# Optimization experiments

Measured on AMD Instinct MI355X. Metric: run time of the kernel, lower is better.

Reference implementation:

```python
import jax, jax.numpy as jnp
import numpy as np

N = 50000
E = 800000
IN_CH = 64
HID = 32
HEADS = 8
OUT_CH = 32
NEG_SLOPE = 0.2  # PyG GATConv default leaky_relu slope


def gat_conv(x, src, dst, W, a_src, a_dst, bias, heads, out_ch, concat, n_nodes):
    # x: [N, F_in]; W: [F_in, heads*out_ch]; a_*: [heads, out_ch]; bias: [heads*out_ch] or [out_ch]
    h = (x @ W).reshape(n_nodes, heads, out_ch)            # [N, H, C]
    alpha_s = jnp.sum(h * a_src, axis=-1)                  # [N, H]
    alpha_d = jnp.sum(h * a_dst, axis=-1)                  # [N, H]
    e = jax.nn.leaky_relu(alpha_s[src] + alpha_d[dst], NEG_SLOPE)  # [E, H]
    # segment softmax over destination node
    m = jax.ops.segment_max(e, dst, num_segments=n_nodes)  # [N, H]
    ex = jnp.exp(e - m[dst])                               # [E, H]
    denom = jax.ops.segment_sum(ex, dst, num_segments=n_nodes)  # [N, H]
    alpha = ex / (denom[dst] + 1e-16)                      # [E, H]
    out = jax.ops.segment_sum(alpha[:, :, None] * h[src], dst, num_segments=n_nodes)  # [N, H, C]
    out = out.reshape(n_nodes, heads * out_ch) if concat else out.mean(axis=1)
    return out + bias


def setup_inputs() -> dict:
    key = jax.random.key(0)
    ks = jax.random.split(key, 12)
    x = jax.random.normal(ks[0], (N, IN_CH), dtype=jnp.float32)
    edge_index = jax.random.randint(ks[1], (2, E), 0, N, dtype=jnp.int32)
    s1 = 1.0 / np.sqrt(IN_CH)
    s2 = 1.0 / np.sqrt(HEADS * HID)
    W1 = jax.random.uniform(ks[2], (IN_CH, HEADS * HID), jnp.float32, -s1, s1)
    a_src1 = jax.random.uniform(ks[3], (HEADS, HID), jnp.float32, -s2, s2)
    a_dst1 = jax.random.uniform(ks[4], (HEADS, HID), jnp.float32, -s2, s2)
    b1 = jnp.zeros((HEADS * HID,), jnp.float32)
    W2 = jax.random.uniform(ks[5], (HEADS * HID, OUT_CH), jnp.float32, -s2, s2)
    a_src2 = jax.random.uniform(ks[6], (1, OUT_CH), jnp.float32, -s2, s2)
    a_dst2 = jax.random.uniform(ks[7], (1, OUT_CH), jnp.float32, -s2, s2)
    b2 = jnp.zeros((OUT_CH,), jnp.float32)
    return {"x": x, "edge_index": edge_index, "W1": W1, "a_src1": a_src1,
            "a_dst1": a_dst1, "b1": b1, "W2": W2, "a_src2": a_src2,
            "a_dst2": a_dst2, "b2": b2}


def reference(x, edge_index, W1, a_src1, a_dst1, b1, W2, a_src2, a_dst2, b2):
    # add self-loops (PyG GATConv default)
    loops = jnp.arange(N, dtype=edge_index.dtype)
    src = jnp.concatenate([edge_index[0], loops])
    dst = jnp.concatenate([edge_index[1], loops])
    h = gat_conv(x, src, dst, W1, a_src1, a_dst1, b1, HEADS, HID, True, N)
    h = jax.nn.relu(h)  # dropout inactive in eval
    out = gat_conv(h, src, dst, W2, a_src2, a_dst2, b2, 1, OUT_CH, False, N)
    return jax.nn.log_softmax(out, axis=1)
```

## Files before the change

### kernel.cpp

```cpp
#include <hip/hip_runtime.h>
#include <math.h>
#include <stdint.h>

#define NN 50000
#define NE 800000
#define INC 64
#define HEADS 8
#define F1 256
#define OC 32
#define NEGS 0.2f

#define NB 391
#define BCAP 2432
#define SCB2 125
#define G1B 1564
#define CSTR 64

typedef unsigned short ushort_t;
typedef float floatx2 __attribute__((ext_vector_type(2)));

__device__ __forceinline__ ushort_t f2bf(float f) {
    uint32_t u = __builtin_bit_cast(uint32_t, f);
    uint32_t r = (u + 0x7fffu + ((u >> 16) & 1u)) >> 16;
    return (ushort_t)r;
}
__device__ __forceinline__ float bflo(uint32_t p) { return __builtin_bit_cast(float, p << 16); }
__device__ __forceinline__ float bfhi(uint32_t p) { return __builtin_bit_cast(float, p & 0xffff0000u); }
__device__ __forceinline__ float bf2f(ushort_t v) { return __builtin_bit_cast(float, (uint32_t)v << 16); }

#if __has_builtin(__builtin_amdgcn_cvt_pk_fp8_f32) && __has_builtin(__builtin_amdgcn_cvt_pk_f32_fp8)
#define HW_FP8 1
#endif

__device__ __forceinline__ uint32_t f2e4m3_sw(float x) {
    float a = fabsf(x);
    uint32_t s = (__builtin_bit_cast(uint32_t, x) >> 31) << 7;
    if (a < 0.015625f) {
        uint32_t m = (uint32_t)rintf(a * 512.0f);
        return s | m;
    }
    if (a >= 448.f) return s | 0x7e;
    uint32_t u = __builtin_bit_cast(uint32_t, a);
    int E = (int)((u >> 23) & 255) - 127;
    float scale = __builtin_bit_cast(float, (uint32_t)(3 - E + 127) << 23);
    uint32_t q = (uint32_t)rintf(a * scale);
    if (q == 16) { E += 1; q = 8; }
    return s | ((uint32_t)(E + 7) << 3) | (q - 8);
}
__device__ __forceinline__ float e4m3f_sw(uint32_t b) {
    uint32_t e = (b >> 3) & 15, m = b & 7;
    float v;
    if (e) v = __builtin_bit_cast(float, ((e + 120u) << 23) | (m << 20));
    else   v = (float)m * 0.001953125f;
    return (b & 0x80u) ? -v : v;
}

__device__ __forceinline__ uint32_t pack4_fp8(float a, float b, float c, float d) {
#ifdef HW_FP8
    int v = __builtin_amdgcn_cvt_pk_fp8_f32(a, b, 0, false);
    v = __builtin_amdgcn_cvt_pk_fp8_f32(c, d, v, true);
    return (uint32_t)v;
#else
    return f2e4m3_sw(a) | (f2e4m3_sw(b) << 8) | (f2e4m3_sw(c) << 16) | (f2e4m3_sw(d) << 24);
#endif
}
__device__ __forceinline__ void unpack4_fp8(uint32_t r, float& f0, float& f1, float& f2, float& f3) {
#ifdef HW_FP8
    floatx2 lo = __builtin_amdgcn_cvt_pk_f32_fp8((int)r, false);
    floatx2 hi = __builtin_amdgcn_cvt_pk_f32_fp8((int)r, true);
    f0 = lo[0]; f1 = lo[1]; f2 = hi[0]; f3 = hi[1];
#else
    f0 = e4m3f_sw(r & 255); f1 = e4m3f_sw((r >> 8) & 255);
    f2 = e4m3f_sw((r >> 16) & 255); f3 = e4m3f_sw(r >> 24);
#endif
}

__global__ __launch_bounds__(256) void k_zero(int* __restrict__ gcnt) {
    int i = blockIdx.x * 256 + threadIdx.x;
    if (i < NB) gcnt[i] = 0;
}

__global__ __launch_bounds__(256) void k_gemm1(
    const float* __restrict__ x, const float* __restrict__ W1,
    const float* __restrict__ a_s, const float* __restrict__ a_d,
    uint8_t* __restrict__ h1, float* __restrict__ alpha_s, float* __restrict__ alpha_d,
    const int* __restrict__ ei, int* __restrict__ gcnt, uint32_t* __restrict__ gbuf)
{
    __shared__ float xt[INC][64];
    __shared__ uint32_t scnt_[NB];
    __shared__ uint32_t soff_[NB];
    int b = blockIdx.x;
    int t = threadIdx.x;

    if (b < SCB2) {
        for (int i = t; i < NB; i += 256) scnt_[i] = 0;
        __syncthreads();
        const int* dsts = ei + NE;
        int ebase = b * 6400;
#pragma unroll
        for (int j = 0; j < 25; ++j) {
            int d = dsts[ebase + j * 256 + t];
            atomicAdd(&scnt_[d >> 7], 1u);
        }
        __syncthreads();
        for (int i = t; i < NB; i += 256) {
            uint32_t c = scnt_[i];
            uint32_t base = 0;
            if (c) base = (uint32_t)atomicAdd(&gcnt[i], (int)c);
            if (base > BCAP) base = BCAP;
            uint32_t end = base + c; if (end > BCAP) end = BCAP;
            soff_[i] = (uint32_t)i * BCAP + base;
            scnt_[i] = (uint32_t)i * BCAP + end;
        }
        __syncthreads();
#pragma unroll
        for (int j = 0; j < 25; ++j) {
            int e = ebase + j * 256 + t;
            int s = ei[e];
            int d = dsts[e];
            int bkt = d >> 7;
            uint32_t slot = atomicAdd(&soff_[bkt], 1u);
            if (slot < scnt_[bkt])
                gbuf[slot] = ((uint32_t)(d & 127) << 16) | (uint32_t)s;
        }
        return;
    }

    int gb = b - SCB2;
    int ntile = gb >> 1;
    int hc = gb & 1;
    int nb = ntile * 64;

    {
        int n = t >> 2;
        int kq = (t & 3) << 4;
        int gn = nb + n;
        if (gn < NN) {
            const float* xr = x + (size_t)gn * INC + kq;
#pragma unroll
            for (int j = 0; j < 16; j += 4) {
                float4 v = *(const float4*)(xr + j);
                xt[kq + j + 0][n] = v.x; xt[kq + j + 1][n] = v.y;
                xt[kq + j + 2][n] = v.z; xt[kq + j + 3][n] = v.w;
            }
        } else {
#pragma unroll
            for (int j = 0; j < 16; ++j) xt[kq + j][n] = 0.f;
        }
    }
    __syncthreads();

    int lane = t & 63, w = t >> 6;
    int ng = lane >> 5;
    int c0 = (lane & 31) << 2;
    int nbase = (w << 4) + (ng << 3);
    int cglob = hc * 128 + c0;
    const float* Wp = W1 + cglob;

    float acc[8][4];
#pragma unroll
    for (int i = 0; i < 8; i++) { acc[i][0] = acc[i][1] = acc[i][2] = acc[i][3] = 0.f; }

#pragma unroll 4
    for (int k = 0; k < INC; ++k) {
        float4 wv = *(const float4*)(Wp + k * F1);
        const float4* xs = (const float4*)&xt[k][nbase];
        float4 xa = xs[0], xb = xs[1];
        float xq[8];
        xq[0] = xa.x; xq[1] = xa.y; xq[2] = xa.z; xq[3] = xa.w;
        xq[4] = xb.x; xq[5] = xb.y; xq[6] = xb.z; xq[7] = xb.w;
#pragma unroll
        for (int ns = 0; ns < 8; ++ns) {
            float xvv = xq[ns];
            acc[ns][0] = fmaf(xvv, wv.x, acc[ns][0]);
            acc[ns][1] = fmaf(xvv, wv.y, acc[ns][1]);
            acc[ns][2] = fmaf(xvv, wv.z, acc[ns][2]);
            acc[ns][3] = fmaf(xvv, wv.w, acc[ns][3]);
        }
    }

    float4 av = *(const float4*)(a_s + cglob);
    float4 dv = *(const float4*)(a_d + cglob);
    int head = hc * 4 + ((lane & 31) >> 3);
#pragma unroll
    for (int ns = 0; ns < 8; ++ns) {
        int n = nb + nbase + ns;
        if (n < NN) {
            uint32_t pk = pack4_fp8(acc[ns][0], acc[ns][1], acc[ns][2], acc[ns][3]);
            *(uint32_t*)(h1 + (size_t)n * F1 + cglob) = pk;
            float ps = acc[ns][0] * av.x + acc[ns][1] * av.y + acc[ns][2] * av.z + acc[ns][3] * av.w;
            float pd = acc[ns][0] * dv.x + acc[ns][1] * dv.y + acc[ns][2] * dv.z + acc[ns][3] * dv.w;
            ps += __shfl_xor(ps, 1); ps += __shfl_xor(ps, 2); ps += __shfl_xor(ps, 4);
            pd += __shfl_xor(pd, 1); pd += __shfl_xor(pd, 2); pd += __shfl_xor(pd, 4);
            if ((lane & 7) == 0) {
                alpha_s[n * HEADS + head] = ps;
                alpha_d[n * HEADS + head] = pd;
            }
        }
    }
}

__global__ __launch_bounds__(256) void k_transpose(
    const int* __restrict__ gcnt, const uint32_t* __restrict__ gbuf,
    ushort_t* __restrict__ csr, int* __restrict__ deg)
{
    __shared__ uint32_t cnt[128], off[128], run[128], sc[128];
    __shared__ ushort_t sent[BCAP];
    int sb = blockIdx.x;
    int t = threadIdx.x;
    if (t < 128) cnt[t] = 0;
    __syncthreads();
    int total = gcnt[sb]; if (total > BCAP) total = BCAP;
    const uint32_t* gb_ = gbuf + (size_t)sb * BCAP;

    for (int i = t; i < total; i += 256) {
        uint32_t v = gb_[i];
        atomicAdd(&cnt[v >> 16], 1u);
    }
    __syncthreads();
    if (t < 128) sc[t] = cnt[t];
    __syncthreads();
    for (int ofs = 1; ofs < 128; ofs <<= 1) {
        uint32_t v = 0;
        if (t < 128 && t >= (uint32_t)ofs) v = sc[t - ofs];
        __syncthreads();
        if (t < 128) sc[t] += v;
        __syncthreads();
    }
    if (t < 128) { off[t] = sc[t] - cnt[t]; run[t] = sc[t] - cnt[t]; }
    __syncthreads();
    for (int i = t; i < total; i += 256) {
        uint32_t v = gb_[i];
        uint32_t slot = atomicAdd(&run[v >> 16], 1u);
        sent[slot] = (ushort_t)(v & 0xffffu);
    }
    __syncthreads();
    int n = t >> 1, half = t & 1;
    int dg = (int)cnt[n];
    if (dg > CSTR) dg = CSTR;
    int d = sb * 128 + n;
    if (half == 0) deg[d] = dg;
    const ushort_t* src = sent + off[n];
    ushort_t* dst = csr + (size_t)d * CSTR;
    for (int j = half; j < dg; j += 2) dst[j] = src[j];
}

__global__ __launch_bounds__(256) void k_gather1(
    const uint8_t* __restrict__ h1,
    const float* __restrict__ alpha_s, const float* __restrict__ alpha_d,
    const int* __restrict__ deg_, const ushort_t* __restrict__ csr,
    const float* __restrict__ b1, uint8_t* __restrict__ h1r8)
{
    int wid = (blockIdx.x * blockDim.x + threadIdx.x) >> 6;
    if (wid >= NN) return;
    int lane = threadIdx.x & 63;
    int d = wid;
    int deg = deg_[d];
    const ushort_t* lst = csr + (size_t)d * CSTR;
    int hh = lane >> 3;
    int he = lane & 7;
    float ad = alpha_d[d * HEADS + hh];
    float ad8 = alpha_d[d * HEADS + he];
    int cb = lane << 2;
    const uint8_t* hbase = h1 + cb;

    float4 A0 = {0.f, 0.f, 0.f, 0.f}, A1 = {0.f, 0.f, 0.f, 0.f};
    float dn0 = 0.f, dn1 = 0.f;

    {
        float e = alpha_s[d * HEADS + hh] + ad;
        uint32_t r = *(const uint32_t*)(hbase + (size_t)d * F1);
        e = (e > 0.f) ? e : NEGS * e;
        float w = __expf(e);
        float f0, f1, f2, f3;
        unpack4_fp8(r, f0, f1, f2, f3);
        dn0 += w;
        A0.x = fmaf(w, f0, A0.x); A0.y = fmaf(w, f1, A0.y);
        A0.z = fmaf(w, f2, A0.z); A0.w = fmaf(w, f3, A0.w);
    }

    int i = 0;
    int je = lane >> 3;
    for (; i + 16 <= deg; i += 16) {
        uint4 pa = *(const uint4*)(lst + i);
        uint4 pb = *(const uint4*)(lst + i + 8);
        uint32_t pwa = (je < 4) ? ((je < 2) ? pa.x : pa.y) : ((je < 6) ? pa.z : pa.w);
        int sa = (je & 1) ? (int)(pwa >> 16) : (int)(pwa & 0xffffu);
        float eoA = alpha_s[sa * HEADS + he] + ad8;
        uint32_t pwb = (je < 4) ? ((je < 2) ? pb.x : pb.y) : ((je < 6) ? pb.z : pb.w);
        int sb_ = (je & 1) ? (int)(pwb >> 16) : (int)(pwb & 0xffffu);
        float eoB = alpha_s[sb_ * HEADS + he] + ad8;
        eoA = (eoA > 0.f) ? eoA : NEGS * eoA;
        eoB = (eoB > 0.f) ? eoB : NEGS * eoB;
        float wA = __expf(eoA);
        float wB = __expf(eoB);
        uint32_t r[16];
        r[0]  = *(const uint32_t*)(hbase + (size_t)(pa.x & 0xffffu) * F1);
        r[1]  = *(const uint32_t*)(hbase + (size_t)(pa.x >> 16) * F1);
        r[2]  = *(const uint32_t*)(hbase + (size_t)(pa.y & 0xffffu) * F1);
        r[3]  = *(const uint32_t*)(hbase + (size_t)(pa.y >> 16) * F1);
        r[4]  = *(const uint32_t*)(hbase + (size_t)(pa.z & 0xffffu) * F1);
        r[5]  = *(const uint32_t*)(hbase + (size_t)(pa.z >> 16) * F1);
        r[6]  = *(const uint32_t*)(hbase + (size_t)(pa.w & 0xffffu) * F1);
        r[7]  = *(const uint32_t*)(hbase + (size_t)(pa.w >> 16) * F1);
        r[8]  = *(const uint32_t*)(hbase + (size_t)(pb.x & 0xffffu) * F1);
        r[9]  = *(const uint32_t*)(hbase + (size_t)(pb.x >> 16) * F1);
        r[10] = *(const uint32_t*)(hbase + (size_t)(pb.y & 0xffffu) * F1);
        r[11] = *(const uint32_t*)(hbase + (size_t)(pb.y >> 16) * F1);
        r[12] = *(const uint32_t*)(hbase + (size_t)(pb.z & 0xffffu) * F1);
        r[13] = *(const uint32_t*)(hbase + (size_t)(pb.z >> 16) * F1);
        r[14] = *(const uint32_t*)(hbase + (size_t)(pb.w & 0xffffu) * F1);
        r[15] = *(const uint32_t*)(hbase + (size_t)(pb.w >> 16) * F1);
#pragma unroll
        for (int j = 0; j < 16; ++j) {
            float w = (j < 8) ? __shfl(wA, (j << 3) + hh)
                              : __shfl(wB, ((j - 8) << 3) + hh);
            float f0, f1, f2, f3;
            unpack4_fp8(r[j], f0, f1, f2, f3);
            if (j & 1) {
                dn1 += w;
                A1.x = fmaf(w, f0, A1.x); A1.y = fmaf(w, f1, A1.y);
                A1.z = fmaf(w, f2, A1.z); A1.w = fmaf(w, f3, A1.w);
            } else {
                dn0 += w;
                A0.x = fmaf(w, f0, A0.x); A0.y = fmaf(w, f1, A0.y);
                A0.z = fmaf(w, f2, A0.z); A0.w = fmaf(w, f3, A0.w);
            }
        }
    }
    for (; i + 8 <= deg; i += 8) {
        uint4 p4 = *(const uint4*)(lst + i);
        uint32_t pw = (je < 4) ? ((je < 2) ? p4.x : p4.y) : ((je < 6) ? p4.z : p4.w);
        int sje = (je & 1) ? (int)(pw >> 16) : (int)(pw & 0xffffu);
        float eo = alpha_s[sje * HEADS + he] + ad8;
        eo = (eo > 0.f) ? eo : NEGS * eo;
        float wown = __expf(eo);
        uint32_t r[8];
        r[0] = *(const uint32_t*)(hbase + (size_t)(p4.x & 0xffffu) * F1);
        r[1] = *(const uint32_t*)(hbase + (size_t)(p4.x >> 16) * F1);
        r[2] = *(const uint32_t*)(hbase + (size_t)(p4.y & 0xffffu) * F1);
        r[3] = *(const uint32_t*)(hbase + (size_t)(p4.y >> 16) * F1);
        r[4] = *(const uint32_t*)(hbase + (size_t)(p4.z & 0xffffu) * F1);
        r[5] = *(const uint32_t*)(hbase + (size_t)(p4.z >> 16) * F1);
        r[6] = *(const uint32_t*)(hbase + (size_t)(p4.w & 0xffffu) * F1);
        r[7] = *(const uint32_t*)(hbase + (size_t)(p4.w >> 16) * F1);
#pragma unroll
        for (int j = 0; j < 8; ++j) {
            float w = __shfl(wown, (j << 3) + hh);
            float f0, f1, f2, f3;
            unpack4_fp8(r[j], f0, f1, f2, f3);
            if (j & 1) {
                dn1 += w;
                A1.x = fmaf(w, f0, A1.x); A1.y = fmaf(w, f1, A1.y);
                A1.z = fmaf(w, f2, A1.z); A1.w = fmaf(w, f3, A1.w);
            } else {
                dn0 += w;
                A0.x = fmaf(w, f0, A0.x); A0.y = fmaf(w, f1, A0.y);
                A0.z = fmaf(w, f2, A0.z); A0.w = fmaf(w, f3, A0.w);
            }
        }
    }
    for (; i + 4 <= deg; i += 4) {
        uint2 p2 = *(const uint2*)(lst + i);
        int s0 = p2.x & 0xffff, s1 = p2.x >> 16, s2 = p2.y & 0xffff, s3 = p2.y >> 16;
        float e0 = alpha_s[s0 * HEADS + hh] + ad;
        float e1 = alpha_s[s1 * HEADS + hh] + ad;
        float e2 = alpha_s[s2 * HEADS + hh] + ad;
        float e3 = alpha_s[s3 * HEADS + hh] + ad;
        uint32_t r0 = *(const uint32_t*)(hbase + (size_t)s0 * F1);
        uint32_t r1 = *(const uint32_t*)(hbase + (size_t)s1 * F1);
        uint32_t r2 = *(const uint32_t*)(hbase + (size_t)s2 * F1);
        uint32_t r3 = *(const uint32_t*)(hbase + (size_t)s3 * F1);
        e0 = (e0 > 0.f) ? e0 : NEGS * e0;
        e1 = (e1 > 0.f) ? e1 : NEGS * e1;
        e2 = (e2 > 0.f) ? e2 : NEGS * e2;
        e3 = (e3 > 0.f) ? e3 : NEGS * e3;
        float w0 = __expf(e0), w1 = __expf(e1), w2 = __expf(e2), w3 = __expf(e3);
        float f0, f1, f2, f3;
        dn0 += w0; dn1 += w1; dn0 += w2; dn1 += w3;
        unpack4_fp8(r0, f0, f1, f2, f3);
        A0.x = fmaf(w0, f0, A0.x); A0.y = fmaf(w0, f1, A0.y);
        A0.z = fmaf(w0, f2, A0.z); A0.w = fmaf(w0, f3, A0.w);
        unpack4_fp8(r1, f0, f1, f2, f3);
        A1.x = fmaf(w1, f0, A1.x); A1.y = fmaf(w1, f1, A1.y);
        A1.z = fmaf(w1, f2, A1.z); A1.w = fmaf(w1, f3, A1.w);
        unpack4_fp8(r2, f0, f1, f2, f3);
        A0.x = fmaf(w2, f0, A0.x); A0.y = fmaf(w2, f1, A0.y);
        A0.z = fmaf(w2, f2, A0.z); A0.w = fmaf(w2, f3, A0.w);
        unpack4_fp8(r3, f0, f1, f2, f3);
        A1.x = fmaf(w3, f0, A1.x); A1.y = fmaf(w3, f1, A1.y);
        A1.z = fmaf(w3, f2, A1.z); A1.w = fmaf(w3, f3, A1.w);
    }
    for (; i < deg; ++i) {
        int s = lst[i];
        float e = alpha_s[s * HEADS + hh] + ad;
        uint32_t r = *(const uint32_t*)(hbase + (size_t)s * F1);
        e = (e > 0.f) ? e : NEGS * e;
        float w = __expf(e);
        float f0, f1, f2, f3;
        unpack4_fp8(r, f0, f1, f2, f3);
        dn0 += w;
        A0.x = fmaf(w, f0, A0.x); A0.y = fmaf(w, f1, A0.y);
        A0.z = fmaf(w, f2, A0.z); A0.w = fmaf(w, f3, A0.w);
    }
    float inv = 1.0f / (dn0 + dn1 + 1e-16f);
    float4 bv = *(const float4*)(b1 + cb);
    uint32_t pk = pack4_fp8(
        fmaxf(fmaf(A0.x + A1.x, inv, bv.x), 0.f),
        fmaxf(fmaf(A0.y + A1.y, inv, bv.y), 0.f),
        fmaxf(fmaf(A0.z + A1.z, inv, bv.z), 0.f),
        fmaxf(fmaf(A0.w + A1.w, inv, bv.w), 0.f));
    *(uint32_t*)(h1r8 + (size_t)d * F1 + cb) = pk;
}

#define G2N 256
#define G2K 16
__global__ __launch_bounds__(256) void k_gemm2(
    const uint8_t* __restrict__ h1r8, const float* __restrict__ W2,
    const float* __restrict__ a_s2, const float* __restrict__ a_d2,
    ushort_t* __restrict__ h2b, float* __restrict__ as2o, float* __restrict__ ad2o)
{
    __shared__ float Wl[F1][OC];
    __shared__ float xt[G2K][G2N];
    int t = threadIdx.x;
    for (int i = t; i < F1 * OC / 4; i += 256)
        ((float4*)Wl)[i] = ((const float4*)W2)[i];
    int nb = blockIdx.x * G2N;
    int lane = t & 63, w = t >> 6;
    int g = lane >> 3, c0 = (lane & 7) << 2;

    float acc[8][4];
#pragma unroll
    for (int i = 0; i < 8; i++) { acc[i][0] = acc[i][1] = acc[i][2] = acc[i][3] = 0.f; }

    for (int kc = 0; kc < F1; kc += G2K) {
        __syncthreads();
        {
            int gn = nb + t;
            if (gn < NN) {
                uint4 v = *(const uint4*)(h1r8 + (size_t)gn * F1 + kc);
                float f0, f1, f2, f3;
                unpack4_fp8(v.x, f0, f1, f2, f3);
                xt[0][t] = f0; xt[1][t] = f1; xt[2][t] = f2; xt[3][t] = f3;
                unpack4_fp8(v.y, f0, f1, f2, f3);
                xt[4][t] = f0; xt[5][t] = f1; xt[6][t] = f2; xt[7][t] = f3;
                unpack4_fp8(v.z, f0, f1, f2, f3);
                xt[8][t] = f0; xt[9][t] = f1; xt[10][t] = f2; xt[11][t] = f3;
                unpack4_fp8(v.w, f0, f1, f2, f3);
                xt[12][t] = f0; xt[13][t] = f1; xt[14][t] = f2; xt[15][t] = f3;
            } else {
#pragma unroll
                for (int kk = 0; kk < G2K; ++kk) xt[kk][t] = 0.f;
            }
        }
        __syncthreads();
        int nbase = (w << 6) + (g << 3);
#pragma unroll
        for (int kk = 0; kk < G2K; ++kk) {
            float4 wv = *(const float4*)&Wl[kc + kk][c0];
            const float4* xs = (const float4*)&xt[kk][nbase];
            float4 xa = xs[0], xb = xs[1];
            float xq[8];
            xq[0] = xa.x; xq[1] = xa.y; xq[2] = xa.z; xq[3] = xa.w;
            xq[4] = xb.x; xq[5] = xb.y; xq[6] = xb.z; xq[7] = xb.w;
#pragma unroll
            for (int ns = 0; ns < 8; ++ns) {
                float xvv = xq[ns];
                acc[ns][0] = fmaf(xvv, wv.x, acc[ns][0]);
                acc[ns][1] = fmaf(xvv, wv.y, acc[ns][1]);
                acc[ns][2] = fmaf(xvv, wv.z, acc[ns][2]);
                acc[ns][3] = fmaf(xvv, wv.w, acc[ns][3]);
            }
        }
    }

    float4 av = *(const float4*)(a_s2 + c0);
    float4 dv = *(const float4*)(a_d2 + c0);
    int nbase2 = nb + (w << 6) + (g << 3);
#pragma unroll
    for (int ns = 0; ns < 8; ++ns) {
        int n = nbase2 + ns;
        if (n < NN) {
            ushort4 pk;
            pk.x = f2bf(acc[ns][0]); pk.y = f2bf(acc[ns][1]);
            pk.z = f2bf(acc[ns][2]); pk.w = f2bf(acc[ns][3]);
            *(ushort4*)(h2b + (size_t)n * OC + c0) = pk;
            float ps = acc[ns][0] * av.x + acc[ns][1] * av.y + acc[ns][2] * av.z + acc[ns][3] * av.w;
            float pd = acc[ns][0] * dv.x + acc[ns][1] * dv.y + acc[ns][2] * dv.z + acc[ns][3] * dv.w;
            ps += __shfl_xor(ps, 1); ps += __shfl_xor(ps, 2); ps += __shfl_xor(ps, 4);
            pd += __shfl_xor(pd, 1); pd += __shfl_xor(pd, 2); pd += __shfl_xor(pd, 4);
            if ((lane & 7) == 0) { as2o[n] = ps; ad2o[n] = pd; }
        }
    }
}

__global__ __launch_bounds__(256) void k_gather2(
    const ushort_t* __restrict__ h2b,
    const float* __restrict__ as2, const float* __restrict__ ad2,
    const int* __restrict__ deg_, const ushort_t* __restrict__ csr,
    const float* __restrict__ b2, float* __restrict__ out)
{
    int wid = (blockIdx.x * blockDim.x + threadIdx.x) >> 6;
    if (wid >= NN) return;
    int lane = threadIdx.x & 63;
    int d = wid;
    int deg = deg_[d];
    const ushort_t* lst = csr + (size_t)d * CSTR;
    int c = lane & 31, half = lane >> 5;
    float ad = ad2[d];
    float ac0 = 0.f, ac1 = 0.f, ac2 = 0.f, ac3 = 0.f;
    float dd0 = 0.f, dd1 = 0.f, dd2 = 0.f, dd3 = 0.f;

    if (half == 0) {
        float e = as2[d] + ad;
        float hv = bf2f(h2b[(size_t)d * OC + c]);
        e = (e > 0.f) ? e : NEGS * e;
        float w = __expf(e);
        dd0 += w;
        ac0 = fmaf(w, hv, ac0);
    }

    int i = half;
    for (; i + 6 < deg; i += 8) {
        int s0 = lst[i];
        int s1 = lst[i + 2];
        int s2 = lst[i + 4];
        int s3 = lst[i + 6];
        float e0 = as2[s0] + ad;
        float e1 = as2[s1] + ad;
        float e2 = as2[s2] + ad;
        float e3 = as2[s3] + ad;
        float h0 = bf2f(h2b[(size_t)s0 * OC + c]);
        float h1v = bf2f(h2b[(size_t)s1 * OC + c]);
        float h2v = bf2f(h2b[(size_t)s2 * OC + c]);
        float h3 = bf2f(h2b[(size_t)s3 * OC + c]);
        e0 = (e0 > 0.f) ? e0 : NEGS * e0;
        e1 = (e1 > 0.f) ? e1 : NEGS * e1;
        e2 = (e2 > 0.f) ? e2 : NEGS * e2;
        e3 = (e3 > 0.f) ? e3 : NEGS * e3;
        float w0 = __expf(e0), w1 = __expf(e1), w2 = __expf(e2), w3 = __expf(e3);
        dd0 += w0; dd1 += w1; dd2 += w2; dd3 += w3;
        ac0 = fmaf(w0, h0, ac0); ac1 = fmaf(w1, h1v, ac1);
        ac2 = fmaf(w2, h2v, ac2); ac3 = fmaf(w3, h3, ac3);
    }
    for (; i < deg; i += 2) {
        int s = lst[i];
        float e = as2[s] + ad;
        float hv = bf2f(h2b[(size_t)s * OC + c]);
        e = (e > 0.f) ? e : NEGS * e;
        float w = __expf(e);
        dd0 += w;
        ac0 = fmaf(w, hv, ac0);
    }
    float acc = (ac0 + ac1) + (ac2 + ac3);
    float denom = (dd0 + dd1) + (dd2 + dd3);
    acc += __shfl_xor(acc, 32);
    denom += __shfl_xor(denom, 32);
    float v = acc / (denom + 1e-16f) + b2[c];
    float m = v;
#pragma unroll
    for (int mm = 1; mm < 32; mm <<= 1) m = fmaxf(m, __shfl_xor(m, mm));
    float ex = __expf(v - m);
    float se = ex;
#pragma unroll
    for (int mm = 1; mm < 32; mm <<= 1) se += __shfl_xor(se, mm);
    float res = v - m - __logf(se);
    if (half == 0) out[(size_t)d * OC + c] = res;
}


extern "C" void kernel_launch(void* const* d_in, const int* in_sizes, int n_in,
                              void* d_out, int out_size, void* d_ws, size_t ws_size,
                              hipStream_t stream) {
    const float* x   = (const float*)d_in[0];
    const int*   ei  = (const int*)d_in[1];
    const float* W1  = (const float*)d_in[2];
    const float* as1 = (const float*)d_in[3];
    const float* ad1 = (const float*)d_in[4];
    const float* b1  = (const float*)d_in[5];
    const float* W2  = (const float*)d_in[6];
    const float* as2 = (const float*)d_in[7];
    const float* ad2 = (const float*)d_in[8];
    const float* b2  = (const float*)d_in[9];
    float* out = (float*)d_out;

    char* p = (char*)d_ws;
    uint8_t*  h1   = (uint8_t*)p;  p += (size_t)NN * F1;
    uint8_t*  h1r8 = (uint8_t*)p;  p += (size_t)NN * F1;
    ushort_t* h2b  = (ushort_t*)p; p += (size_t)NN * OC * 2;
    float* a_s1 = (float*)p; p += (size_t)NN * HEADS * 4;
    float* a_d1 = (float*)p; p += (size_t)NN * HEADS * 4;
    float* a_s2 = (float*)p; p += (size_t)NN * 4;
    float* a_d2 = (float*)p; p += (size_t)NN * 4;
    int* gcnt = (int*)p; p += (size_t)((NB + 7) & ~7) * 4;
    uint32_t* gbuf = (uint32_t*)p; p += (size_t)NB * BCAP * 4;
    ushort_t* csr = (ushort_t*)p; p += (size_t)(NB * 128) * CSTR * 2;
    int* deg = (int*)p; p += (size_t)(NB * 128) * 4;

    k_zero<<<(NB + 255) / 256, 256, 0, stream>>>(gcnt);

    k_gemm1<<<SCB2 + G1B, 256, 0, stream>>>(x, W1, as1, ad1, h1, a_s1, a_d1,
                                            ei, gcnt, gbuf);

    k_transpose<<<NB, 256, 0, stream>>>(gcnt, gbuf, csr, deg);

    int gwblocks = (NN + 3) / 4;
    k_gather1<<<gwblocks, 256, 0, stream>>>(h1, a_s1, a_d1, deg, csr, b1, h1r8);

    int g2blocks = (NN + G2N - 1) / G2N;
    k_gemm2<<<g2blocks, 256, 0, stream>>>(h1r8, W2, as2, ad2, h2b, a_s2, a_d2);

    k_gather2<<<gwblocks, 256, 0, stream>>>(h2b, a_s2, a_d2, deg, csr, b2, out);
}
```

Measured before the change: 151.7 us.

## Split layer-1 gather wavefront into two half-waves over edges with 8-byte row loads

The layer-1 aggregation kernel now splits each 64-lane wavefront into two 32-lane halves. Each half processes a different subset of neighbor edges, and each lane loads 8 fp8 features (uint2) instead of 4. The halves are combined at the end with cross-lane xor shuffles. This removes the per-edge weight shuffles and doubles the bytes per gather load, which should cut instruction count and improve memory-level parallelism. In exchange each lane recomputes the exp for its head, and the 32-way shuffle reduction plus the odd-degree tail handling add some overhead.

```diff
diff --git a/kernel.cpp b/kernel.cpp
--- a/kernel.cpp
+++ b/kernel.cpp
@@ -257,160 +257,133 @@
     int d = wid;
     int deg = deg_[d];
     const ushort_t* lst = csr + (size_t)d * CSTR;
-    int hh = lane >> 3;
-    int he = lane & 7;
-    float ad = alpha_d[d * HEADS + hh];
-    float ad8 = alpha_d[d * HEADS + he];
-    int cb = lane << 2;
-    const uint8_t* hbase = h1 + cb;
-
-    float4 A0 = {0.f, 0.f, 0.f, 0.f}, A1 = {0.f, 0.f, 0.f, 0.f};
-    float dn0 = 0.f, dn1 = 0.f;
-
-    {
-        float e = alpha_s[d * HEADS + hh] + ad;
-        uint32_t r = *(const uint32_t*)(hbase + (size_t)d * F1);
+    int l5 = lane & 31, half = lane >> 5;
+    int hd = l5 >> 2;
+    int cb8 = l5 << 3;
+    float ad = alpha_d[d * HEADS + hd];
+    const uint8_t* hb = h1 + cb8;
+
+    float A0 = 0.f, A1 = 0.f, A2 = 0.f, A3 = 0.f;
+    float A4 = 0.f, A5 = 0.f, A6 = 0.f, A7 = 0.f;
+    float dn = 0.f;
+
+#define G1_ACC(RXY, W)  { float f0,f1,f2,f3,f4,f5,f6,f7; \
+    unpack4_fp8((RXY).x, f0,f1,f2,f3); unpack4_fp8((RXY).y, f4,f5,f6,f7); \
+    A0 = fmaf(W,f0,A0); A1 = fmaf(W,f1,A1); A2 = fmaf(W,f2,A2); A3 = fmaf(W,f3,A3); \
+    A4 = fmaf(W,f4,A4); A5 = fmaf(W,f5,A5); A6 = fmaf(W,f6,A6); A7 = fmaf(W,f7,A7); }
+
+    if (half == 0) {
+        float e = alpha_s[d * HEADS + hd] + ad;
+        uint2 r = *(const uint2*)(hb + (size_t)d * F1);
         e = (e > 0.f) ? e : NEGS * e;
         float w = __expf(e);
-        float f0, f1, f2, f3;
-        unpack4_fp8(r, f0, f1, f2, f3);
-        dn0 += w;
-        A0.x = fmaf(w, f0, A0.x); A0.y = fmaf(w, f1, A0.y);
-        A0.z = fmaf(w, f2, A0.z); A0.w = fmaf(w, f3, A0.w);
+        dn += w;
+        G1_ACC(r, w)
     }
 
     int i = 0;
-    int je = lane >> 3;
     for (; i + 16 <= deg; i += 16) {
-        uint4 pa = *(const uint4*)(lst + i);
-        uint4 pb = *(const uint4*)(lst + i + 8);
-        uint32_t pwa = (je < 4) ? ((je < 2) ? pa.x : pa.y) : ((je < 6) ? pa.z : pa.w);
-        int sa = (je & 1) ? (int)(pwa >> 16) : (int)(pwa & 0xffffu);
-        float eoA = alpha_s[sa * HEADS + he] + ad8;
-        uint32_t pwb = (je < 4) ? ((je < 2) ? pb.x : pb.y) : ((je < 6) ? pb.z : pb.w);
-        int sb_ = (je & 1) ? (int)(pwb >> 16) : (int)(pwb & 0xffffu);
-        float eoB = alpha_s[sb_ * HEADS + he] + ad8;
-        eoA = (eoA > 0.f) ? eoA : NEGS * eoA;
-        eoB = (eoB > 0.f) ? eoB : NEGS * eoB;
-        float wA = __expf(eoA);
-        float wB = __expf(eoB);
-        uint32_t r[16];
-        r[0]  = *(const uint32_t*)(hbase + (size_t)(pa.x & 0xffffu) * F1);
-        r[1]  = *(const uint32_t*)(hbase + (size_t)(pa.x >> 16) * F1);
-        r[2]  = *(const uint32_t*)(hbase + (size_t)(pa.y & 0xffffu) * F1);
-        r[3]  = *(const uint32_t*)(hbase + (size_t)(pa.y >> 16) * F1);
-        r[4]  = *(const uint32_t*)(hbase + (size_t)(pa.z & 0xffffu) * F1);
-        r[5]  = *(const uint32_t*)(hbase + (size_t)(pa.z >> 16) * F1);
-        r[6]  = *(const uint32_t*)(hbase + (size_t)(pa.w & 0xffffu) * F1);
-        r[7]  = *(const uint32_t*)(hbase + (size_t)(pa.w >> 16) * F1);
-        r[8]  = *(const uint32_t*)(hbase + (size_t)(pb.x & 0xffffu) * F1);
-        r[9]  = *(const uint32_t*)(hbase + (size_t)(pb.x >> 16) * F1);
-        r[10] = *(const uint32_t*)(hbase + (size_t)(pb.y & 0xffffu) * F1);
-        r[11] = *(const uint32_t*)(hbase + (size_t)(pb.y >> 16) * F1);
-        r[12] = *(const uint32_t*)(hbase + (size_t)(pb.z & 0xffffu) * F1);
-        r[13] = *(const uint32_t*)(hbase + (size_t)(pb.z >> 16) * F1);
-        r[14] = *(const uint32_t*)(hbase + (size_t)(pb.w & 0xffffu) * F1);
-        r[15] = *(const uint32_t*)(hbase + (size_t)(pb.w >> 16) * F1);
-#pragma unroll
-        for (int j = 0; j < 16; ++j) {
-            float w = (j < 8) ? __shfl(wA, (j << 3) + hh)
-                              : __shfl(wB, ((j - 8) << 3) + hh);
-            float f0, f1, f2, f3;
-            unpack4_fp8(r[j], f0, f1, f2, f3);
-            if (j & 1) {
-                dn1 += w;
-                A1.x = fmaf(w, f0, A1.x); A1.y = fmaf(w, f1, A1.y);
-                A1.z = fmaf(w, f2, A1.z); A1.w = fmaf(w, f3, A1.w);
-            } else {
-                dn0 += w;
-                A0.x = fmaf(w, f0, A0.x); A0.y = fmaf(w, f1, A0.y);
-                A0.z = fmaf(w, f2, A0.z); A0.w = fmaf(w, f3, A0.w);
-            }
-        }
+        uint4 p4 = *(const uint4*)(lst + i + (half << 3));
+        int s0 = p4.x & 0xffff, s1 = p4.x >> 16;
+        int s2 = p4.y & 0xffff, s3 = p4.y >> 16;
+        int s4 = p4.z & 0xffff, s5 = p4.z >> 16;
+        int s6 = p4.w & 0xffff, s7 = p4.w >> 16;
+        float e0 = alpha_s[s0 * HEADS + hd];
+        float e1 = alpha_s[s1 * HEADS + hd];
+        float e2 = alpha_s[s2 * HEADS + hd];
+        float e3 = alpha_s[s3 * HEADS + hd];
+        float e4 = alpha_s[s4 * HEADS + hd];
+        float e5 = alpha_s[s5 * HEADS + hd];
+        float e6 = alpha_s[s6 * HEADS + hd];
+        float e7 = alpha_s[s7 * HEADS + hd];
+        uint2 r0 = *(const uint2*)(hb + (size_t)s0 * F1);
+        uint2 r1 = *(const uint2*)(hb + (size_t)s1 * F1);
+        uint2 r2 = *(const uint2*)(hb + (size_t)s2 * F1);
+        uint2 r3 = *(const uint2*)(hb + (size_t)s3 * F1);
+        uint2 r4 = *(const uint2*)(hb + (size_t)s4 * F1);
+        uint2 r5 = *(const uint2*)(hb + (size_t)s5 * F1);
+        uint2 r6 = *(const uint2*)(hb + (size_t)s6 * F1);
+        uint2 r7 = *(const uint2*)(hb + (size_t)s7 * F1);
+        e0 += ad; e1 += ad; e2 += ad; e3 += ad;
+        e4 += ad; e5 += ad; e6 += ad; e7 += ad;
+        e0 = (e0 > 0.f) ? e0 : NEGS * e0;
+        e1 = (e1 > 0.f) ? e1 : NEGS * e1;
+        e2 = (e2 > 0.f) ? e2 : NEGS * e2;
+        e3 = (e3 > 0.f) ? e3 : NEGS * e3;
+        e4 = (e4 > 0.f) ? e4 : NEGS * e4;
+        e5 = (e5 > 0.f) ? e5 : NEGS * e5;
+        e6 = (e6 > 0.f) ? e6 : NEGS * e6;
+        e7 = (e7 > 0.f) ? e7 : NEGS * e7;
+        float w0 = __expf(e0), w1 = __expf(e1), w2 = __expf(e2), w3 = __expf(e3);
+        float w4 = __expf(e4), w5 = __expf(e5), w6 = __expf(e6), w7 = __expf(e7);
+        dn += w0 + w1 + w2 + w3 + w4 + w5 + w6 + w7;
+        G1_ACC(r0, w0) G1_ACC(r1, w1) G1_ACC(r2, w2) G1_ACC(r3, w3)
+        G1_ACC(r4, w4) G1_ACC(r5, w5) G1_ACC(r6, w6) G1_ACC(r7, w7)
     }
     for (; i + 8 <= deg; i += 8) {
-        uint4 p4 = *(const uint4*)(lst + i);
-        uint32_t pw = (je < 4) ? ((je < 2) ? p4.x : p4.y) : ((je < 6) ? p4.z : p4.w);
-        int sje = (je & 1) ? (int)(pw >> 16) : (int)(pw & 0xffffu);
-        float eo = alpha_s[sje * HEADS + he] + ad8;
-        eo = (eo > 0.f) ? eo : NEGS * eo;
-        float wown = __expf(eo);
-        uint32_t r[8];
-        r[0] = *(const uint32_t*)(hbase + (size_t)(p4.x & 0xffffu) * F1);
-        r[1] = *(const uint32_t*)(hbase + (size_t)(p4.x >> 16) * F1);
-        r[2] = *(const uint32_t*)(hbase + (size_t)(p4.y & 0xffffu) * F1);
-        r[3] = *(const uint32_t*)(hbase + (size_t)(p4.y >> 16) * F1);
-        r[4] = *(const uint32_t*)(hbase + (size_t)(p4.z & 0xffffu) * F1);
-        r[5] = *(const uint32_t*)(hbase + (size_t)(p4.z >> 16) * F1);
-        r[6] = *(const uint32_t*)(hbase + (size_t)(p4.w & 0xffffu) * F1);
-        r[7] = *(const uint32_t*)(hbase + (size_t)(p4.w >> 16) * F1);
-#pragma unroll
-        for (int j = 0; j < 8; ++j) {
-            float w = __shfl(wown, (j << 3) + hh);
-            float f0, f1, f2, f3;
-            unpack4_fp8(r[j], f0, f1, f2, f3);
-            if (j & 1) {
-                dn1 += w;
-                A1.x = fmaf(w, f0, A1.x); A1.y = fmaf(w, f1, A1.y);
-                A1.z = fmaf(w, f2, A1.z); A1.w = fmaf(w, f3, A1.w);
-            } else {
-                dn0 += w;
-                A0.x = fmaf(w, f0, A0.x); A0.y = fmaf(w, f1, A0.y);
-                A0.z = fmaf(w, f2, A0.z); A0.w = fmaf(w, f3, A0.w);
-            }
-        }
-    }
-    for (; i + 4 <= deg; i += 4) {
-        uint2 p2 = *(const uint2*)(lst + i);
-        int s0 = p2.x & 0xffff, s1 = p2.x >> 16, s2 = p2.y & 0xffff, s3 = p2.y >> 16;
-        float e0 = alpha_s[s0 * HEADS + hh] + ad;
-        float e1 = alpha_s[s1 * HEADS + hh] + ad;
-        float e2 = alpha_s[s2 * HEADS + hh] + ad;
-        float e3 = alpha_s[s3 * HEADS + hh] + ad;
-        uint32_t r0 = *(const uint32_t*)(hbase + (size_t)s0 * F1);
-        uint32_t r1 = *(const uint32_t*)(hbase + (size_t)s1 * F1);
-        uint32_t r2 = *(const uint32_t*)(hbase + (size_t)s2 * F1);
-        uint32_t r3 = *(const uint32_t*)(hbase + (size_t)s3 * F1);
+        uint2 p2 = *(const uint2*)(lst + i + (half << 2));
+        int s0 = p2.x & 0xffff, s1 = p2.x >> 16;
+        int s2 = p2.y & 0xffff, s3 = p2.y >> 16;
+        float e0 = alpha_s[s0 * HEADS + hd];
+        float e1 = alpha_s[s1 * HEADS + hd];
+        float e2 = alpha_s[s2 * HEADS + hd];
+        float e3 = alpha_s[s3 * HEADS + hd];
+        uint2 r0 = *(const uint2*)(hb + (size_t)s0 * F1);
+        uint2 r1 = *(const uint2*)(hb + (size_t)s1 * F1);
+        uint2 r2 = *(const uint2*)(hb + (size_t)s2 * F1);
+        uint2 r3 = *(const uint2*)(hb + (size_t)s3 * F1);
+        e0 += ad; e1 += ad; e2 += ad; e3 += ad;
         e0 = (e0 > 0.f) ? e0 : NEGS * e0;
         e1 = (e1 > 0.f) ? e1 : NEGS * e1;
         e2 = (e2 > 0.f) ? e2 : NEGS * e2;
         e3 = (e3 > 0.f) ? e3 : NEGS * e3;
         float w0 = __expf(e0), w1 = __expf(e1), w2 = __expf(e2), w3 = __expf(e3);
-        float f0, f1, f2, f3;
-        dn0 += w0; dn1 += w1; dn0 += w2; dn1 += w3;
-        unpack4_fp8(r0, f0, f1, f2, f3);
-        A0.x = fmaf(w0, f0, A0.x); A0.y = fmaf(w0, f1, A0.y);
-        A0.z = fmaf(w0, f2, A0.z); A0.w = fmaf(w0, f3, A0.w);
-        unpack4_fp8(r1, f0, f1, f2, f3);
-        A1.x = fmaf(w1, f0, A1.x); A1.y = fmaf(w1, f1, A1.y);
-        A1.z = fmaf(w1, f2, A1.z); A1.w = fmaf(w1, f3, A1.w);
-        unpack4_fp8(r2, f0, f1, f2, f3);
-        A0.x = fmaf(w2, f0, A0.x); A0.y = fmaf(w2, f1, A0.y);
-        A0.z = fmaf(w2, f2, A0.z); A0.w = fmaf(w2, f3, A0.w);
-        unpack4_fp8(r3, f0, f1, f2, f3);
-        A1.x = fmaf(w3, f0, A1.x); A1.y = fmaf(w3, f1, A1.y);
-        A1.z = fmaf(w3, f2, A1.z); A1.w = fmaf(w3, f3, A1.w);
-    }
-    for (; i < deg; ++i) {
-        int s = lst[i];
-        float e = alpha_s[s * HEADS + hh] + ad;
-        uint32_t r = *(const uint32_t*)(hbase + (size_t)s * F1);
+        dn += w0 + w1 + w2 + w3;
+        G1_ACC(r0, w0) G1_ACC(r1, w1) G1_ACC(r2, w2) G1_ACC(r3, w3)
+    }
+    for (; i + 2 <= deg; i += 2) {
+        int s = lst[i + half];
+        float e = alpha_s[s * HEADS + hd] + ad;
+        uint2 r = *(const uint2*)(hb + (size_t)s * F1);
         e = (e > 0.f) ? e : NEGS * e;
         float w = __expf(e);
-        float f0, f1, f2, f3;
-        unpack4_fp8(r, f0, f1, f2, f3);
-        dn0 += w;
-        A0.x = fmaf(w, f0, A0.x); A0.y = fmaf(w, f1, A0.y);
-        A0.z = fmaf(w, f2, A0.z); A0.w = fmaf(w, f3, A0.w);
-    }
-    float inv = 1.0f / (dn0 + dn1 + 1e-16f);
-    float4 bv = *(const float4*)(b1 + cb);
-    uint32_t pk = pack4_fp8(
-        fmaxf(fmaf(A0.x + A1.x, inv, bv.x), 0.f),
-        fmaxf(fmaf(A0.y + A1.y, inv, bv.y), 0.f),
-        fmaxf(fmaf(A0.z + A1.z, inv, bv.z), 0.f),
-        fmaxf(fmaf(A0.w + A1.w, inv, bv.w), 0.f));
-    *(uint32_t*)(h1r8 + (size_t)d * F1 + cb) = pk;
+        dn += w;
+        G1_ACC(r, w)
+    }
+    if (i < deg && half == 0) {
+        int s = lst[i];
+        float e = alpha_s[s * HEADS + hd] + ad;
+        uint2 r = *(const uint2*)(hb + (size_t)s * F1);
+        e = (e > 0.f) ? e : NEGS * e;
+        float w = __expf(e);
+        dn += w;
+        G1_ACC(r, w)
+    }
+#undef G1_ACC
+
+    dn += __shfl_xor(dn, 32);
+    A0 += __shfl_xor(A0, 32); A1 += __shfl_xor(A1, 32);
+    A2 += __shfl_xor(A2, 32); A3 += __shfl_xor(A3, 32);
+    A4 += __shfl_xor(A4, 32); A5 += __shfl_xor(A5, 32);
+    A6 += __shfl_xor(A6, 32); A7 += __shfl_xor(A7, 32);
+
+    if (half == 0) {
+        float inv = 1.0f / (dn + 1e-16f);
+        float4 bv0 = *(const float4*)(b1 + cb8);
+        float4 bv1 = *(const float4*)(b1 + cb8 + 4);
+        uint2 o;
+        o.x = pack4_fp8(
+            fmaxf(fmaf(A0, inv, bv0.x), 0.f),
+            fmaxf(fmaf(A1, inv, bv0.y), 0.f),
+            fmaxf(fmaf(A2, inv, bv0.z), 0.f),
+            fmaxf(fmaf(A3, inv, bv0.w), 0.f));
+        o.y = pack4_fp8(
+            fmaxf(fmaf(A4, inv, bv1.x), 0.f),
+            fmaxf(fmaf(A5, inv, bv1.y), 0.f),
+            fmaxf(fmaf(A6, inv, bv1.z), 0.f),
+            fmaxf(fmaf(A7, inv, bv1.w), 0.f));
+        *(uint2*)(h1r8 + (size_t)d * F1 + cb8) = o;
+    }
 }
 
 #define G2N 256
```

After: 148.9 us. No clear change (-1.9%).
